# Performance work log

Hardware: AMD Instinct MI355X
Metric: run time of the kernel (lower is better)

The kernel has to match this reference:

```python
import jax, jax.numpy as jnp
import numpy as np

NUM_HEADS = 8
NUM_Q = 64
RANK = 64
DIM = 768
LN_EPS = 1e-5


def setup_inputs() -> dict:
    key = jax.random.key(0)
    ks = jax.random.split(key, 8)
    b, n = 4, 1024
    x = jax.random.normal(ks[0], (b, NUM_Q, DIM), dtype=jnp.float32)
    context = jax.random.normal(ks[1], (b, n, DIM), dtype=jnp.float32)
    s = 0.02
    Wq = jax.random.normal(ks[2], (DIM, DIM), dtype=jnp.float32) * s
    Wk = jax.random.normal(ks[3], (DIM, DIM), dtype=jnp.float32) * s
    Wv1 = jax.random.normal(ks[4], (DIM, NUM_Q * RANK), dtype=jnp.float32) * s
    ln_g = jnp.ones((NUM_Q * RANK,), dtype=jnp.float32)
    ln_b = jnp.zeros((NUM_Q * RANK,), dtype=jnp.float32)
    Wc = jax.random.normal(ks[5], (NUM_Q, RANK, DIM), dtype=jnp.float32) * s
    Wout = jax.random.normal(ks[6], (DIM, DIM), dtype=jnp.float32) * s
    return {"x": x, "context": context, "Wq": Wq, "Wk": Wk, "Wv1": Wv1,
            "ln_g": ln_g, "ln_b": ln_b, "Wc": Wc, "Wout": Wout}


def reference(x, context, Wq, Wk, Wv1, ln_g, ln_b, Wc, Wout):
    b, nq, d = x.shape
    n = context.shape[1]
    h, dh = NUM_HEADS, d // NUM_HEADS

    q = x @ Wq                      # [b, nq, d]
    k = context @ Wk                # [b, n, d]

    # q-aware V: Linear -> LayerNorm(all_q_mid) -> grouped 1x1 conv (per-query rank->d)
    h1 = context @ Wv1              # [b, n, NUM_Q*RANK]
    mu = jnp.mean(h1, axis=-1, keepdims=True)
    var = jnp.var(h1, axis=-1, keepdims=True)
    h1 = (h1 - mu) * jax.lax.rsqrt(var + LN_EPS) * ln_g + ln_b
    vmid = h1.reshape(b, n, NUM_Q, RANK)
    v = jnp.einsum('bnqr,qrd->bqnd', vmid, Wc)   # [b, NUM_Q, n, d]
    # split heads: 'b q n (h dh) -> b h q n dh'
    v = v.reshape(b, NUM_Q, n, h, dh).transpose(0, 3, 1, 2, 4)

    qh = q.reshape(b, nq, h, dh).transpose(0, 2, 1, 3)   # [b,h,nq,dh]
    kh = k.reshape(b, n, h, dh).transpose(0, 2, 1, 3)    # [b,h,n,dh]
    scale = dh ** (-0.25)
    sim = jnp.einsum('bhid,bhjd->bhij', qh * scale, kh * scale)
    attn = jax.nn.softmax(sim, axis=-1)                  # [b,h,nq,n]
    out = jnp.einsum('bhij,bhijd->bhid', attn, v)        # per-query V
    out = out.transpose(0, 2, 1, 3).reshape(b, nq, d)
    return out @ Wout
```

## Files before the change

### kernel.cpp

```cpp
#include <hip/hip_runtime.h>
#include <math.h>

typedef unsigned short ushort_t;
typedef __bf16 bf16x8 __attribute__((ext_vector_type(8)));
typedef float f32x4 __attribute__((ext_vector_type(4)));

__device__ __forceinline__ ushort_t f2b_rne(float f) {
    union { float f; unsigned int u; } c;
    c.f = f;
    unsigned int u = c.u;
    u += 0x7FFFu + ((u >> 16) & 1u);
    return (ushort_t)(u >> 16);
}
__device__ __forceinline__ float b2f(ushort_t v) {
    union { unsigned int u; float f; } c;
    c.u = ((unsigned int)v) << 16;
    return c.f;
}

__device__ __forceinline__ void gl_lds16(const ushort_t* g, ushort_t* l) {
    __builtin_amdgcn_global_load_lds(
        (const __attribute__((address_space(1))) void*)g,
        (__attribute__((address_space(3))) void*)l, 16, 0, 0);
}

__global__ __launch_bounds__(256) void prep(
    const float* __restrict__ x, const float* __restrict__ context,
    const float* __restrict__ Wq, const float* __restrict__ Wk,
    const float* __restrict__ Wv1, const float* __restrict__ Wout,
    ushort_t* __restrict__ x_b, ushort_t* __restrict__ ctx_b,
    ushort_t* __restrict__ Wq_t, ushort_t* __restrict__ Wk_t,
    ushort_t* __restrict__ Wv1_t, ushort_t* __restrict__ Wout_b,
    float* __restrict__ colzero,
    int b, int n) {
    const int t = threadIdx.x;
    const int bid = blockIdx.x;
    const int nb_x = (b * 64 * 768 / 4) / 256;
    const int nb_c = (b * n * 768 / 4) / 256;

    if (bid < nb_x + nb_c) {
        const float* in = (bid < nb_x) ? x : context;
        ushort_t* outp = (bid < nb_x) ? x_b : ctx_b;
        const int i = ((bid < nb_x) ? bid : (bid - nb_x)) * 256 + t;
        float4 v = ((const float4*)in)[i];
        ushort_t o[4] = {f2b_rne(v.x), f2b_rne(v.y), f2b_rne(v.z), f2b_rne(v.w)};
        *(uint2*)&outp[(size_t)i * 4] = *(uint2*)o;
        return;
    }

    int u = bid - nb_x - nb_c;
    if (u >= 1632) {
        const int idx = (u - 1632) * 256 + t;
        ((float4*)colzero)[idx] = make_float4(0.f, 0.f, 0.f, 0.f);
        return;
    }
    if (u >= 1056) {
        const int i = (u - 1056) * 256 + t;
        float4 v = ((const float4*)Wout)[i];
        ushort_t o[4] = {f2b_rne(v.x), f2b_rne(v.y), f2b_rne(v.z), f2b_rne(v.w)};
        *(uint2*)&Wout_b[(size_t)i * 4] = *(uint2*)o;
        return;
    }

    const float* in;
    ushort_t* outp;
    int R = 768, C = 768;
    if (u < 144)        { in = Wq;  outp = Wq_t; }
    else if (u < 288)   { u -= 144; in = Wk;  outp = Wk_t; }
    else                { u -= 288; in = Wv1; outp = Wv1_t; C = 4096; }
    const int ct = C / 64;
    const int c0 = (u % ct) * 64, r0 = (u / ct) * 64;

    __shared__ float tt[64][65];
    const int lr = t >> 4;
    const int lc = (t & 15) * 4;
#pragma unroll
    for (int i = 0; i < 4; i++) {
        const float4 v =
            *(const float4*)&in[(size_t)(r0 + lr + 16 * i) * C + c0 + lc];
        tt[lr + 16 * i][lc + 0] = v.x;
        tt[lr + 16 * i][lc + 1] = v.y;
        tt[lr + 16 * i][lc + 2] = v.z;
        tt[lr + 16 * i][lc + 3] = v.w;
    }
    __syncthreads();
    const int rr = (t & 15) * 4;
    const int cc = t >> 4;
#pragma unroll
    for (int i = 0; i < 4; i++) {
        const int col = cc + 16 * i;
        ushort_t o[4] = {f2b_rne(tt[rr + 0][col]), f2b_rne(tt[rr + 1][col]),
                         f2b_rne(tt[rr + 2][col]), f2b_rne(tt[rr + 3][col])};
        *(uint2*)&outp[(size_t)(c0 + col) * R + r0 + rr] = *(uint2*)o;
    }
}

__device__ __forceinline__ void gemm_tile_big(
    const ushort_t* __restrict__ A, const ushort_t* __restrict__ Bt,
    ushort_t* __restrict__ C, int N, int row0, int col0, ushort_t* lds) {
    constexpr int K = 768;
    constexpr int NSTEP = 24;
    constexpr int SLOT = 512 * 32;

    const int t = threadIdx.x;
    const int lane = t & 63, wave = t >> 6;
    const int quad = lane >> 4, l15 = lane & 15;
    const int wm = (wave >> 2) * 128;
    const int wn = (wave & 3) * 64;

    const int srow = lane >> 2;
    const int sslot = (lane & 3) ^ ((lane >> 3) & 3);
    const ushort_t* gA = A + (size_t)(row0 + wave * 32 + srow) * K + sslot * 8;
    const ushort_t* gB = Bt + (size_t)(col0 + wave * 32 + srow) * K + sslot * 8;
    const int ldsA = wave * 1024;
    const int ldsB = 256 * 32 + wave * 1024;

    const int rslot = (quad ^ ((l15 >> 1) & 3)) * 8;
    const int abase = (wm + l15) * 32 + rslot;
    const int bbase = 256 * 32 + (wn + l15) * 32 + rslot;

    f32x4 acc[8][4] = {};
    bf16x8 af[8], bfr[4];

    auto STAGE_A = [&](int s) {
        const int rg = (s & 3) * SLOT;
        const int ko = s * 32;
        gl_lds16(gA + ko, lds + rg + ldsA);
        gl_lds16(gA + 16 * K + ko, lds + rg + ldsA + 512);
    };
    auto STAGE_B = [&](int s) {
        const int rg = (s & 3) * SLOT;
        const int ko = s * 32;
        gl_lds16(gB + ko, lds + rg + ldsB);
        gl_lds16(gB + 16 * K + ko, lds + rg + ldsB + 512);
    };
    auto READ_B = [&](int s) {
        const ushort_t* p = lds + (s & 3) * SLOT + bbase;
#pragma unroll
        for (int j = 0; j < 4; ++j) bfr[j] = *(const bf16x8*)&p[j * 512];
    };
    auto READ_A_LO = [&](int s) {
        const ushort_t* p = lds + (s & 3) * SLOT + abase;
#pragma unroll
        for (int i = 0; i < 4; ++i) af[i] = *(const bf16x8*)&p[i * 512];
    };
    auto READ_A_HI = [&](int s) {
        const ushort_t* p = lds + (s & 3) * SLOT + abase;
#pragma unroll
        for (int i = 4; i < 8; ++i) af[i] = *(const bf16x8*)&p[i * 512];
    };
    auto MFMA_LO = [&]() {
        __builtin_amdgcn_s_setprio(1);
#pragma unroll
        for (int i = 0; i < 4; ++i)
#pragma unroll
            for (int j = 0; j < 4; ++j)
                acc[i][j] = __builtin_amdgcn_mfma_f32_16x16x32_bf16(
                    af[i], bfr[j], acc[i][j], 0, 0, 0);
        __builtin_amdgcn_s_setprio(0);
    };
    auto MFMA_HI = [&]() {
        __builtin_amdgcn_s_setprio(1);
#pragma unroll
        for (int i = 4; i < 8; ++i)
#pragma unroll
            for (int j = 0; j < 4; ++j)
                acc[i][j] = __builtin_amdgcn_mfma_f32_16x16x32_bf16(
                    af[i], bfr[j], acc[i][j], 0, 0, 0);
        __builtin_amdgcn_s_setprio(0);
    };

    STAGE_A(0); STAGE_B(0);
    STAGE_A(1); STAGE_B(1);
    STAGE_A(2); STAGE_B(2);
    asm volatile("s_waitcnt vmcnt(8)" ::: "memory");
    __builtin_amdgcn_s_barrier();

    for (int s = 0; s < NSTEP - 3; ++s) {
        READ_B(s);
        READ_A_LO(s);
        STAGE_A(s + 3);
        __builtin_amdgcn_sched_barrier(0);
        __builtin_amdgcn_s_barrier();
        asm volatile("s_waitcnt lgkmcnt(0)" ::: "memory");
        __builtin_amdgcn_sched_barrier(0);
        MFMA_LO();
        __builtin_amdgcn_sched_barrier(0);
        __builtin_amdgcn_s_barrier();
        READ_A_HI(s);
        STAGE_B(s + 3);
        asm volatile("s_waitcnt vmcnt(8)" ::: "memory");
        __builtin_amdgcn_sched_barrier(0);
        __builtin_amdgcn_s_barrier();
        asm volatile("s_waitcnt lgkmcnt(0)" ::: "memory");
        __builtin_amdgcn_sched_barrier(0);
        MFMA_HI();
        __builtin_amdgcn_sched_barrier(0);
        __builtin_amdgcn_s_barrier();
    }

    asm volatile("s_waitcnt vmcnt(0)" ::: "memory");
    __builtin_amdgcn_s_barrier();
#pragma unroll
    for (int s = NSTEP - 3; s < NSTEP; ++s) {
        READ_B(s);
        READ_A_LO(s);
        READ_A_HI(s);
        asm volatile("s_waitcnt lgkmcnt(0)" ::: "memory");
        __builtin_amdgcn_sched_barrier(0);
        MFMA_LO();
        MFMA_HI();
    }

#pragma unroll
    for (int i = 0; i < 8; ++i)
#pragma unroll
        for (int j = 0; j < 4; ++j)
#pragma unroll
            for (int r = 0; r < 4; ++r) {
                const int row = row0 + wm + i * 16 + quad * 4 + r;
                const int col = col0 + wn + j * 16 + l15;
                C[(size_t)row * N + col] = f2b_rne(acc[i][j][r]);
            }
}

__device__ __forceinline__ void gemm_tile_small(
    const ushort_t* __restrict__ A, const ushort_t* __restrict__ Bt,
    ushort_t* __restrict__ C, int N, int row0, int col0, ushort_t* lds) {
    constexpr int K = 768;
    constexpr int NSTEP = 24;
    constexpr int SLOT = 256 * 32;

    const int t = threadIdx.x;
    const int lane = t & 63, wave = t >> 6;
    const int quad = lane >> 4, l15 = lane & 15;
    const int wm = (wave >> 2) * 64;
    const int wn = (wave & 3) * 32;

    const int srow = lane >> 2;
    const int sslot = (lane & 3) ^ ((lane >> 3) & 3);
    const ushort_t* gA = A + (size_t)(row0 + wave * 16 + srow) * K + sslot * 8;
    const ushort_t* gB = Bt + (size_t)(col0 + wave * 16 + srow) * K + sslot * 8;
    const int ldsA = wave * 512;
    const int ldsB = 128 * 32 + wave * 512;

    const int rslot = (quad ^ ((l15 >> 1) & 3)) * 8;
    const int abase = (wm + l15) * 32 + rslot;
    const int bbase = 128 * 32 + (wn + l15) * 32 + rslot;

    f32x4 acc[4][2] = {};

    auto STAGE = [&](int s) {
        const int rg = (s & 3) * SLOT;
        const int ko = s * 32;
        gl_lds16(gA + ko, lds + rg + ldsA);
        gl_lds16(gB + ko, lds + rg + ldsB);
    };

    auto COMPUTE = [&](int s) {
        const int rg = (s & 3) * SLOT;
        const ushort_t* pA = lds + rg + abase;
        const ushort_t* pB = lds + rg + bbase;
        bf16x8 af[4], bfr[2];
#pragma unroll
        for (int i = 0; i < 4; ++i) af[i] = *(const bf16x8*)&pA[i * 512];
#pragma unroll
        for (int j = 0; j < 2; ++j) bfr[j] = *(const bf16x8*)&pB[j * 512];
        __builtin_amdgcn_s_setprio(1);
#pragma unroll
        for (int i = 0; i < 4; ++i)
#pragma unroll
            for (int j = 0; j < 2; ++j)
                acc[i][j] = __builtin_amdgcn_mfma_f32_16x16x32_bf16(
                    af[i], bfr[j], acc[i][j], 0, 0, 0);
        __builtin_amdgcn_s_setprio(0);
    };

    STAGE(0); STAGE(1); STAGE(2);

    for (int s = 0; s < NSTEP - 3; ++s) {
        __builtin_amdgcn_sched_barrier(0);
        __builtin_amdgcn_s_barrier();
        STAGE(s + 3);
        asm volatile("s_waitcnt vmcnt(6)" ::: "memory");
        __builtin_amdgcn_s_barrier();
        __builtin_amdgcn_sched_barrier(0);
        COMPUTE(s);
    }
    __builtin_amdgcn_sched_barrier(0);
    __builtin_amdgcn_s_barrier();
    asm volatile("s_waitcnt vmcnt(0)" ::: "memory");
    __builtin_amdgcn_s_barrier();
    __builtin_amdgcn_sched_barrier(0);
    COMPUTE(NSTEP - 3);
    COMPUTE(NSTEP - 2);
    COMPUTE(NSTEP - 1);

#pragma unroll
    for (int i = 0; i < 4; ++i)
#pragma unroll
        for (int j = 0; j < 2; ++j)
#pragma unroll
            for (int r = 0; r < 4; ++r) {
                const int row = row0 + wm + i * 16 + quad * 4 + r;
                const int col = col0 + wn + j * 16 + l15;
                C[(size_t)row * N + col] = f2b_rne(acc[i][j][r]);
            }
}

__global__ __launch_bounds__(512, 2) void gemm_ring(
    const ushort_t* __restrict__ x_b, const ushort_t* __restrict__ ctx_b,
    const ushort_t* __restrict__ Wq_t, const ushort_t* __restrict__ Wk_t,
    const ushort_t* __restrict__ Wv1_t,
    ushort_t* __restrict__ qb, ushort_t* __restrict__ kb,
    ushort_t* __restrict__ h1t, int b, int n) {
    extern __shared__ ushort_t lds[];
    const int Mn = b * n;
    const int M = b * 64;
    const int nbig = 16 * (Mn / 256);
    const int nk = (Mn / 128) * 6;
    int u = blockIdx.x;
    if (u < nbig) {
        gemm_tile_big(Wv1_t, ctx_b, h1t, Mn, (u & 15) * 256, (u >> 4) * 256,
                      lds);
    } else if ((u -= nbig) < nk) {
        const int rt = Mn / 128;
        gemm_tile_small(ctx_b, Wk_t, kb, 768, (u % rt) * 128, (u / rt) * 128,
                        lds);
    } else {
        u -= nk;
        const int rt = M / 128;
        gemm_tile_small(x_b, Wq_t, qb, 768, (u % rt) * 128, (u / rt) * 128,
                        lds);
    }
}

__global__ __launch_bounds__(256) void scores_stats(
    const ushort_t* __restrict__ qb, const ushort_t* __restrict__ kb,
    const ushort_t* __restrict__ h1t, float* __restrict__ S,
    float* __restrict__ colsum, float* __restrict__ colsumsq,
    int b, int n, int Mn) {
    __shared__ ushort_t sb[192 * 104];
    const int t = threadIdx.x;
    const int nsc = b * 8 * (n / 128);

    if (blockIdx.x >= nsc) {
        const int u = blockIdx.x - nsc;
        const int rc = u >> 4;
        const int cc = u & 15;
        const int cg = t & 31;
        const int rg = t >> 5;
        const ushort_t* p =
            h1t + (size_t)(rc * 256 + rg * 32) * Mn + cc * 256 + cg * 8;
        float s[8] = {}, s2[8] = {};
#pragma unroll 4
        for (int r = 0; r < 32; r++) {
            const bf16x8 v = *(const bf16x8*)&p[(size_t)r * Mn];
#pragma unroll
            for (int j = 0; j < 8; j++) {
                const float f = (float)v[j];
                s[j] += f;
                s2[j] += f * f;
            }
        }
        float* red = (float*)sb;
#pragma unroll
        for (int j = 0; j < 8; j++) {
            red[rg * 256 + cg * 8 + j] = s[j];
            red[2048 + rg * 256 + cg * 8 + j] = s2[j];
        }
        __syncthreads();
        float ts = 0.f, ts2 = 0.f;
#pragma unroll
        for (int g = 0; g < 8; g++) {
            ts += red[g * 256 + t];
            ts2 += red[2048 + g * 256 + t];
        }
        atomicAdd(&colsum[cc * 256 + t], ts);
        atomicAdd(&colsumsq[cc * 256 + t], ts2);
        return;
    }

    const int nt = n / 128;
    const int n0 = (blockIdx.x % nt) * 128;
    const int bh = blockIdx.x / nt;
    const int bb = bh >> 3, h = bh & 7;
    const int lane = t & 63, wave = t >> 6;
    const int quad = lane >> 4, l15 = lane & 15;
    const int wm = (wave >> 1) * 32;
    const int wn = (wave & 1) * 64;

    ushort_t* Qs = sb;
    ushort_t* Ks = sb + 64 * 104;

    for (int g = t; g < 768; g += 256) {
        const int r = g / 12, s = g - r * 12;
        *(bf16x8*)&Qs[r * 104 + s * 8] =
            *(const bf16x8*)&qb[(size_t)(bb * 64 + r) * 768 + h * 96 + s * 8];
    }
    for (int g = t; g < 1536; g += 256) {
        const int r = g / 12, s = g - r * 12;
        *(bf16x8*)&Ks[r * 104 + s * 8] =
            *(const bf16x8*)&kb[(size_t)(bb * n + n0 + r) * 768 + h * 96 + s * 8];
    }
    __syncthreads();

    f32x4 acc[2][4] = {};
#pragma unroll
    for (int ks = 0; ks < 3; ks++) {
        bf16x8 af[2], bfr[4];
#pragma unroll
        for (int i = 0; i < 2; i++)
            af[i] = *(const bf16x8*)&Qs[(wm + i * 16 + l15) * 104 + ks * 32 + quad * 8];
#pragma unroll
        for (int j = 0; j < 4; j++)
            bfr[j] = *(const bf16x8*)&Ks[(wn + j * 16 + l15) * 104 + ks * 32 + quad * 8];
#pragma unroll
        for (int i = 0; i < 2; i++)
#pragma unroll
            for (int j = 0; j < 4; j++)
                acc[i][j] = __builtin_amdgcn_mfma_f32_16x16x32_bf16(
                    af[i], bfr[j], acc[i][j], 0, 0, 0);
    }

    const float sc = 0.10206207261596575f;
    float* Sp = S + (size_t)bh * 64 * n;
#pragma unroll
    for (int i = 0; i < 2; i++)
#pragma unroll
        for (int j = 0; j < 4; j++)
#pragma unroll
            for (int r = 0; r < 4; r++) {
                const int row = wm + i * 16 + quad * 4 + r;
                const int col = n0 + wn + j * 16 + l15;
                Sp[(size_t)row * n + col] = acc[i][j][r] * sc;
            }
}

__global__ __launch_bounds__(1024) void attn_fused(
    const float* __restrict__ S, const float* __restrict__ colsum,
    const float* __restrict__ colsumsq, const ushort_t* __restrict__ h1t,
    const float* __restrict__ ln_g, const float* __restrict__ ln_b,
    const float* __restrict__ Wc, const ushort_t* __restrict__ Wout_b,
    float* __restrict__ out, int n, int Mn) {
    const int bq = blockIdx.x;
    const int bb = bq >> 6, qi = bq & 63;
    const int tid = threadIdx.x;
    const int lane = tid & 63, wv = tid >> 6;
    const int quad = lane >> 4, l15 = lane & 15;

    __shared__ ushort_t sW[9 * 1032];
    __shared__ ushort_t sH[64 * 264];
    __shared__ float sl[8], swmu[8];
    __shared__ float pm[16], pl[16], pwm[16];
    __shared__ float sA[512];
    __shared__ float sO[768];

    float* sMu = (float*)sH;
    float* sRs = (float*)sH + 1024;

    for (int i = tid; i < n; i += 1024) {
        const float cs = colsum[bb * n + i];
        const float cq = colsumsq[bb * n + i];
        const float m = cs * (1.0f / 4096.0f);
        sMu[i] = m;
        sRs[i] = rsqrtf(cq * (1.0f / 4096.0f) - m * m + 1e-5f);
    }
    for (int i = tid; i < 1032; i += 1024) sW[8 * 1032 + i] = 0;
    __syncthreads();

    const int h = wv >> 1;
    const int half = wv & 1;
    const int nh = n >> 1;
    const int i0 = half * nh;
    const float* Sp = S + ((size_t)(bb * 8 + h) * 64 + qi) * n;
    float l = 0.f, wmacc = 0.f;
    if (nh == 512) {
        float sv[8];
        {
            float m = -1e30f;
#pragma unroll
            for (int k = 0; k < 8; k++) {
                sv[k] = Sp[i0 + lane + k * 64];
                m = fmaxf(m, sv[k]);
            }
#pragma unroll
            for (int off = 32; off > 0; off >>= 1)
                m = fmaxf(m, __shfl_down(m, off));
            if (lane == 0) pm[wv] = m;
        }
        __syncthreads();
        const float mh = fmaxf(pm[2 * h], pm[2 * h + 1]);
#pragma unroll
        for (int k = 0; k < 8; k++) {
            const int i = i0 + lane + k * 64;
            const float e = expf(sv[k] - mh);
            const float w = e * sRs[i];
            const ushort_t wb = f2b_rne(w);
            sW[h * 1032 + i] = wb;
            l += e;
            wmacc += b2f(wb) * sMu[i];
        }
    } else {
        {
            float m = -1e30f;
            for (int i = i0 + lane; i < i0 + nh; i += 64) m = fmaxf(m, Sp[i]);
#pragma unroll
            for (int off = 32; off > 0; off >>= 1)
                m = fmaxf(m, __shfl_down(m, off));
            if (lane == 0) pm[wv] = m;
        }
        __syncthreads();
        const float mh = fmaxf(pm[2 * h], pm[2 * h + 1]);
        for (int i = i0 + lane; i < i0 + nh; i += 64) {
            const float e = expf(Sp[i] - mh);
            const float w = e * sRs[i];
            const ushort_t wb = f2b_rne(w);
            sW[h * 1032 + i] = wb;
            l += e;
            wmacc += b2f(wb) * sMu[i];
        }
    }
#pragma unroll
    for (int off = 32; off > 0; off >>= 1) {
        l += __shfl_down(l, off);
        wmacc += __shfl_down(wmacc, off);
    }
    if (lane == 0) { pl[wv] = l; pwm[wv] = wmacc; }
    __syncthreads();
    if (tid < 8) {
        sl[tid] = pl[2 * tid] + pl[2 * tid + 1];
        swmu[tid] = pwm[2 * tid] + pwm[2 * tid + 1];
    }

    const int mrow = (l15 < 8 ? l15 : 8) * 1032;
    const int jb = wv & 3;
    const int kg = wv >> 2;
    f32x4 acc = {};
    {
        const ushort_t* hp =
            h1t + (size_t)(qi * 64 + jb * 16 + l15) * Mn + bb * n + kg * 256 +
            quad * 8;
        const ushort_t* wp = sW + mrow + kg * 256 + quad * 8;
#pragma unroll
        for (int ks = 0; ks < 8; ks++) {
            const bf16x8 af = *(const bf16x8*)&wp[ks * 32];
            const bf16x8 bf = *(const bf16x8*)&hp[ks * 32];
            acc = __builtin_amdgcn_mfma_f32_16x16x32_bf16(af, bf, acc, 0, 0, 0);
        }
    }
    __syncthreads();
    float* red = (float*)sH;
    *(f32x4*)&red[(size_t)(wv * 64 + lane) * 4] = acc;
    __syncthreads();

    if (wv < 4) {
        f32x4 a = *(const f32x4*)&red[(size_t)(wv * 64 + lane) * 4];
#pragma unroll
        for (int g = 1; g < 4; g++) {
            const f32x4 p = *(const f32x4*)&red[(size_t)((g * 4 + wv) * 64 + lane) * 4];
#pragma unroll
            for (int r = 0; r < 4; r++) a[r] += p[r];
        }
#pragma unroll
        for (int r = 0; r < 4; r++) {
            const int hh = quad * 4 + r;
            if (hh < 8) {
                const int rr = wv * 16 + l15;
                const int c = qi * 64 + rr;
                sA[hh * 64 + rr] =
                    ln_g[c] * ((a[r] - swmu[hh]) / sl[hh]) + ln_b[c];
            }
        }
    }
    __syncthreads();

    for (int d = tid; d < 768; d += 1024) {
        const int hh = d / 96;
        const float* wp = Wc + (size_t)qi * 49152 + d;
        float a = 0.f;
#pragma unroll
        for (int r = 0; r < 64; r++) a += sA[hh * 64 + r] * wp[(size_t)r * 768];
        sO[d] = b2f(f2b_rne(a));
    }
    __syncthreads();

    float* rbuf = (float*)sH;
    if (tid < 768) {
        const int r0 = tid / 96;
        const int c0 = (tid % 96) * 8;
        const ushort_t* wp = Wout_b + (size_t)(r0 * 96) * 768 + c0;
        float acc8[8] = {};
#pragma unroll 4
        for (int s = 0; s < 96; s++) {
            const float sv = sO[r0 * 96 + s];
            const bf16x8 w8 = *(const bf16x8*)&wp[(size_t)s * 768];
#pragma unroll
            for (int j = 0; j < 8; j++) acc8[j] += sv * (float)w8[j];
        }
#pragma unroll
        for (int j = 0; j < 8; j++) rbuf[r0 * 768 + c0 + j] = acc8[j];
    }
    __syncthreads();
    if (tid < 768) {
        float s = 0.f;
#pragma unroll
        for (int g = 0; g < 8; g++) s += rbuf[g * 768 + tid];
        out[(size_t)bq * 768 + tid] = s;
    }
}

extern "C" void kernel_launch(void* const* d_in, const int* in_sizes, int n_in,
                              void* d_out, int out_size, void* d_ws, size_t ws_size,
                              hipStream_t stream) {
    const float* x       = (const float*)d_in[0];
    const float* context = (const float*)d_in[1];
    const float* Wq      = (const float*)d_in[2];
    const float* Wk      = (const float*)d_in[3];
    const float* Wv1     = (const float*)d_in[4];
    const float* ln_g    = (const float*)d_in[5];
    const float* ln_b    = (const float*)d_in[6];
    const float* Wc      = (const float*)d_in[7];
    const float* Wout    = (const float*)d_in[8];
    float* out = (float*)d_out;

    const int b = in_sizes[0] / (64 * 768);
    const int n = in_sizes[1] / (b * 768);
    const int M  = b * 64;
    const int Mn = b * n;

    float* ws = (float*)d_ws;
    size_t off = 0;
    float* S       = ws + off;  off += (size_t)b * 8 * 64 * n;
    float* colsum  = ws + off;  off += (size_t)Mn;
    float* colsumsq= ws + off;  off += (size_t)Mn;

    ushort_t* us = (ushort_t*)(ws + off);
    size_t uo = 0;
    ushort_t* x_b    = us + uo;  uo += (size_t)M * 768;
    ushort_t* ctx_b  = us + uo;  uo += (size_t)Mn * 768;
    ushort_t* qb     = us + uo;  uo += (size_t)M * 768;
    ushort_t* kb     = us + uo;  uo += (size_t)Mn * 768;
    ushort_t* h1t    = us + uo;  uo += (size_t)Mn * 4096;
    ushort_t* Wq_t   = us + uo;  uo += (size_t)768 * 768;
    ushort_t* Wk_t   = us + uo;  uo += (size_t)768 * 768;
    ushort_t* Wv1_t  = us + uo;  uo += (size_t)4096 * 768;
    ushort_t* Wout_b = us + uo;  uo += (size_t)768 * 768;

    const int nb_x = (M * 768 / 4) / 256;
    const int nb_c = (Mn * 768 / 4) / 256;
    prep<<<nb_x + nb_c + 1640, 256, 0, stream>>>(
        x, context, Wq, Wk, Wv1, Wout, x_b, ctx_b, Wq_t, Wk_t, Wv1_t, Wout_b,
        colsum, b, n);

    const int nbig = 16 * (Mn / 256);
    const int nk = (Mn / 128) * 6;
    const int nq = (M / 128) * 6;
    static bool attr_done = false;
    if (!attr_done) {
        (void)hipFuncSetAttribute(reinterpret_cast<const void*>(&gemm_ring),
                                  hipFuncAttributeMaxDynamicSharedMemorySize,
                                  131072);
        attr_done = true;
    }
    gemm_ring<<<nbig + nk + nq, 512, 131072, stream>>>(
        x_b, ctx_b, Wq_t, Wk_t, Wv1_t, qb, kb, h1t, b, n);

    scores_stats<<<b * 8 * (n / 128) + 256, 256, 0, stream>>>(
        qb, kb, h1t, S, colsum, colsumsq, b, n, Mn);

    attn_fused<<<M, 1024, 0, stream>>>(S, colsum, colsumsq, h1t, ln_g, ln_b,
                                       Wc, Wout_b, out, n, Mn);
}
```

Measured before the change: 165.7 us.

## Move final Wout projection from attn_fused into a separate MFMA GEMM kernel

The per-row scalar Wout matvec at the end of attn_fused is removed. attn_fused now writes a bf16 intermediate, and a new out_gemm kernel runs the reusable MFMA tile GEMM with an fp32 output path against a transposed Wout prepared in prep. This replaces 256 blocks that each streamed the full bf16 Wout with one tensor-core GEMM, shortening attn_fused. The cost is an extra launch, an extra intermediate round-trip through global memory, and a small GEMM (M=256) that gives only 12 blocks.

```diff
diff --git a/kernel.cpp b/kernel.cpp
--- a/kernel.cpp
+++ b/kernel.cpp
@@ -30,7 +30,7 @@
     const float* __restrict__ Wv1, const float* __restrict__ Wout,
     ushort_t* __restrict__ x_b, ushort_t* __restrict__ ctx_b,
     ushort_t* __restrict__ Wq_t, ushort_t* __restrict__ Wk_t,
-    ushort_t* __restrict__ Wv1_t, ushort_t* __restrict__ Wout_b,
+    ushort_t* __restrict__ Wv1_t, ushort_t* __restrict__ Wout_t,
     float* __restrict__ colzero,
     int b, int n) {
     const int t = threadIdx.x;
@@ -49,25 +49,19 @@
     }
 
     int u = bid - nb_x - nb_c;
-    if (u >= 1632) {
-        const int idx = (u - 1632) * 256 + t;
+    if (u >= 1200) {
+        const int idx = (u - 1200) * 256 + t;
         ((float4*)colzero)[idx] = make_float4(0.f, 0.f, 0.f, 0.f);
-        return;
-    }
-    if (u >= 1056) {
-        const int i = (u - 1056) * 256 + t;
-        float4 v = ((const float4*)Wout)[i];
-        ushort_t o[4] = {f2b_rne(v.x), f2b_rne(v.y), f2b_rne(v.z), f2b_rne(v.w)};
-        *(uint2*)&Wout_b[(size_t)i * 4] = *(uint2*)o;
         return;
     }
 
     const float* in;
     ushort_t* outp;
     int R = 768, C = 768;
-    if (u < 144)        { in = Wq;  outp = Wq_t; }
-    else if (u < 288)   { u -= 144; in = Wk;  outp = Wk_t; }
-    else                { u -= 288; in = Wv1; outp = Wv1_t; C = 4096; }
+    if (u < 144)        { in = Wq;   outp = Wq_t; }
+    else if (u < 288)   { u -= 144;  in = Wk;   outp = Wk_t; }
+    else if (u < 432)   { u -= 288;  in = Wout; outp = Wout_t; }
+    else                { u -= 432;  in = Wv1;  outp = Wv1_t; C = 4096; }
     const int ct = C / 64;
     const int c0 = (u % ct) * 64, r0 = (u / ct) * 64;
 
@@ -224,9 +218,10 @@
             }
 }
 
+template <bool OUT_F32>
 __device__ __forceinline__ void gemm_tile_small(
     const ushort_t* __restrict__ A, const ushort_t* __restrict__ Bt,
-    ushort_t* __restrict__ C, int N, int row0, int col0, ushort_t* lds) {
+    void* __restrict__ Cv, int N, int row0, int col0, ushort_t* lds) {
     constexpr int K = 768;
     constexpr int NSTEP = 24;
     constexpr int SLOT = 256 * 32;
@@ -304,7 +299,11 @@
             for (int r = 0; r < 4; ++r) {
                 const int row = row0 + wm + i * 16 + quad * 4 + r;
                 const int col = col0 + wn + j * 16 + l15;
-                C[(size_t)row * N + col] = f2b_rne(acc[i][j][r]);
+                if constexpr (OUT_F32)
+                    ((float*)Cv)[(size_t)row * N + col] = acc[i][j][r];
+                else
+                    ((ushort_t*)Cv)[(size_t)row * N + col] =
+                        f2b_rne(acc[i][j][r]);
             }
 }
 
@@ -325,14 +324,23 @@
                       lds);
     } else if ((u -= nbig) < nk) {
         const int rt = Mn / 128;
-        gemm_tile_small(ctx_b, Wk_t, kb, 768, (u % rt) * 128, (u / rt) * 128,
-                        lds);
+        gemm_tile_small<false>(ctx_b, Wk_t, kb, 768, (u % rt) * 128,
+                               (u / rt) * 128, lds);
     } else {
         u -= nk;
         const int rt = M / 128;
-        gemm_tile_small(x_b, Wq_t, qb, 768, (u % rt) * 128, (u / rt) * 128,
-                        lds);
-    }
+        gemm_tile_small<false>(x_b, Wq_t, qb, 768, (u % rt) * 128,
+                               (u / rt) * 128, lds);
+    }
+}
+
+__global__ __launch_bounds__(512, 2) void out_gemm(
+    const ushort_t* __restrict__ oA, const ushort_t* __restrict__ Wout_t,
+    float* __restrict__ out, int M) {
+    extern __shared__ ushort_t lds[];
+    const int rt = M / 128;
+    gemm_tile_small<true>(oA, Wout_t, out, 768, (blockIdx.x % rt) * 128,
+                          (blockIdx.x / rt) * 128, lds);
 }
 
 __global__ __launch_bounds__(256) void scores_stats(
@@ -441,8 +449,8 @@
     const float* __restrict__ S, const float* __restrict__ colsum,
     const float* __restrict__ colsumsq, const ushort_t* __restrict__ h1t,
     const float* __restrict__ ln_g, const float* __restrict__ ln_b,
-    const float* __restrict__ Wc, const ushort_t* __restrict__ Wout_b,
-    float* __restrict__ out, int n, int Mn) {
+    const float* __restrict__ Wc, ushort_t* __restrict__ oA,
+    int n, int Mn) {
     const int bq = blockIdx.x;
     const int bb = bq >> 6, qi = bq & 63;
     const int tid = threadIdx.x;
@@ -454,7 +462,6 @@
     __shared__ float sl[8], swmu[8];
     __shared__ float pm[16], pl[16], pwm[16];
     __shared__ float sA[512];
-    __shared__ float sO[768];
 
     float* sMu = (float*)sH;
     float* sRs = (float*)sH + 1024;
@@ -575,38 +582,14 @@
     }
     __syncthreads();
 
-    for (int d = tid; d < 768; d += 1024) {
+    if (tid < 768) {
+        const int d = tid;
         const int hh = d / 96;
         const float* wp = Wc + (size_t)qi * 49152 + d;
         float a = 0.f;
 #pragma unroll
         for (int r = 0; r < 64; r++) a += sA[hh * 64 + r] * wp[(size_t)r * 768];
-        sO[d] = b2f(f2b_rne(a));
-    }
-    __syncthreads();
-
-    float* rbuf = (float*)sH;
-    if (tid < 768) {
-        const int r0 = tid / 96;
-        const int c0 = (tid % 96) * 8;
-        const ushort_t* wp = Wout_b + (size_t)(r0 * 96) * 768 + c0;
-        float acc8[8] = {};
-#pragma unroll 4
-        for (int s = 0; s < 96; s++) {
-            const float sv = sO[r0 * 96 + s];
-            const bf16x8 w8 = *(const bf16x8*)&wp[(size_t)s * 768];
-#pragma unroll
-            for (int j = 0; j < 8; j++) acc8[j] += sv * (float)w8[j];
-        }
-#pragma unroll
-        for (int j = 0; j < 8; j++) rbuf[r0 * 768 + c0 + j] = acc8[j];
-    }
-    __syncthreads();
-    if (tid < 768) {
-        float s = 0.f;
-#pragma unroll
-        for (int g = 0; g < 8; g++) s += rbuf[g * 768 + tid];
-        out[(size_t)bq * 768 + tid] = s;
+        oA[(size_t)bq * 768 + d] = f2b_rne(a);
     }
 }
 
@@ -645,12 +628,13 @@
     ushort_t* Wq_t   = us + uo;  uo += (size_t)768 * 768;
     ushort_t* Wk_t   = us + uo;  uo += (size_t)768 * 768;
     ushort_t* Wv1_t  = us + uo;  uo += (size_t)4096 * 768;
-    ushort_t* Wout_b = us + uo;  uo += (size_t)768 * 768;
+    ushort_t* Wout_t = us + uo;  uo += (size_t)768 * 768;
+    ushort_t* oA     = us + uo;  uo += (size_t)M * 768;
 
     const int nb_x = (M * 768 / 4) / 256;
     const int nb_c = (Mn * 768 / 4) / 256;
-    prep<<<nb_x + nb_c + 1640, 256, 0, stream>>>(
-        x, context, Wq, Wk, Wv1, Wout, x_b, ctx_b, Wq_t, Wk_t, Wv1_t, Wout_b,
+    prep<<<nb_x + nb_c + 1208, 256, 0, stream>>>(
+        x, context, Wq, Wk, Wv1, Wout, x_b, ctx_b, Wq_t, Wk_t, Wv1_t, Wout_t,
         colsum, b, n);
 
     const int nbig = 16 * (Mn / 256);
@@ -661,6 +645,9 @@
         (void)hipFuncSetAttribute(reinterpret_cast<const void*>(&gemm_ring),
                                   hipFuncAttributeMaxDynamicSharedMemorySize,
                                   131072);
+        (void)hipFuncSetAttribute(reinterpret_cast<const void*>(&out_gemm),
+                                  hipFuncAttributeMaxDynamicSharedMemorySize,
+                                  65536);
         attr_done = true;
     }
     gemm_ring<<<nbig + nk + nq, 512, 131072, stream>>>(
@@ -670,5 +657,7 @@
         qb, kb, h1t, S, colsum, colsumsq, b, n, Mn);
 
     attn_fused<<<M, 1024, 0, stream>>>(S, colsum, colsumsq, h1t, ln_g, ln_b,
-                                       Wc, Wout_b, out, n, Mn);
-}
+                                       Wc, oA, n, Mn);
+
+    out_gemm<<<(M / 128) * 6, 512, 65536, stream>>>(oA, Wout_t, out, M);
+}
```

Result: no change. 166.5 us (+0.5%).
